# Kernel tuning notes

Hardware: AMD Instinct MI355X
Metric: run time of the kernel (lower is better)

## Reference

```python
import jax, jax.numpy as jnp
import numpy as np

HEADS = 4


def setup_inputs() -> dict:
    key = jax.random.key(0)
    k1, k2, k3, k4 = jax.random.split(key, 4)
    B, C, H, W = 4, 256, 64, 64
    x = jax.random.normal(k1, (B, C, H, W), dtype=jnp.float32)
    w_qkv = jax.random.normal(k2, (3 * C, C), dtype=jnp.float32) * (C ** -0.5)
    w_proj = jax.random.normal(k3, (C, C), dtype=jnp.float32) * (C ** -0.5)
    b_proj = jax.random.normal(k4, (C,), dtype=jnp.float32) * 0.01
    return {"x": x, "w_qkv": w_qkv, "w_proj": w_proj, "b_proj": b_proj}


def reference(x, w_qkv, w_proj, b_proj):
    B, C, H, W = x.shape
    heads = HEADS
    dh = C // heads
    scale = dh ** -0.5
    N = H * W
    # 1x1 conv == channel matmul
    qkv = jnp.einsum('bchw,oc->bohw', x, w_qkv)  # [B, 3C, H, W]
    q, k, v = jnp.split(qkv, 3, axis=1)          # each [B, C, H, W]

    def rs(t):
        # [B, C, H, W] -> [B, heads, N, dh]
        return t.reshape(B, heads, dh, N).transpose(0, 1, 3, 2)

    q, k, v = rs(q), rs(k), rs(v)
    attn = jax.nn.softmax(jnp.einsum('bhnd,bhmd->bhnm', q, k) * scale, axis=-1)
    out = jnp.einsum('bhnm,bhmd->bhnd', attn, v)        # [B, heads, N, dh]
    out = out.transpose(0, 1, 3, 2).reshape(B, C, H, W)  # back to spatial
    return jnp.einsum('bchw,oc->bohw', out, w_proj) + b_proj[None, :, None, None]
```

## Files before the change

kernel.cpp:

```cpp
#include <hip/hip_runtime.h>
#include <hip/hip_bf16.h>

#define NPOS   4096
#define TOTP   16384
#define C      256
#define DH     64

typedef unsigned short ushort_t;
typedef __attribute__((ext_vector_type(8))) short short8;
typedef __attribute__((ext_vector_type(4))) float f32x4;

__device__ __forceinline__ f32x4 mfma16(short8 a, short8 b, f32x4 c) {
  return __builtin_amdgcn_mfma_f32_16x16x32_bf16(a, b, c, 0, 0, 0);
}

__device__ __forceinline__ ushort_t f2bf(float f) {
  union { float f; unsigned int u; } v;
  v.f = f;
  unsigned int r = v.u + 0x7FFFu + ((v.u >> 16) & 1u);
  return (ushort_t)(r >> 16);
}

__device__ __forceinline__ unsigned int pack_bf16x2(float lo, float hi) {
  __hip_bfloat162 h = __float22bfloat162_rn(float2{lo, hi});
  union { __hip_bfloat162 h; unsigned int u; } v;
  v.h = h;
  return v.u;
}

__device__ __forceinline__ float fast_exp2(float x) {
  float r;
  asm("v_exp_f32 %0, %1" : "=v"(r) : "v"(x));
  return r;
}

__global__ __launch_bounds__(256) void pack_w(const float* __restrict__ wq,
                                              const float* __restrict__ wp,
                                              ushort_t* __restrict__ wqb,
                                              ushort_t* __restrict__ wpb) {
  int idx = blockIdx.x * 256 + threadIdx.x;
  if (idx < 49152) {
    float4 v = *(const float4*)(wq + (size_t)idx * 4);
    float sc = (idx * 4 < 65536) ? 0.18033688f : 1.0f;
    ushort_t* d = wqb + (size_t)idx * 4;
    unsigned long long pk =
        (unsigned long long)f2bf(v.x * sc) |
        ((unsigned long long)f2bf(v.y * sc) << 16) |
        ((unsigned long long)f2bf(v.z * sc) << 32) |
        ((unsigned long long)f2bf(v.w * sc) << 48);
    *(unsigned long long*)d = pk;
  } else {
    int j = idx - 49152;
    float4 v = *(const float4*)(wp + (size_t)j * 4);
    ushort_t* d = wpb + (size_t)j * 4;
    unsigned long long pk =
        (unsigned long long)f2bf(v.x) |
        ((unsigned long long)f2bf(v.y) << 16) |
        ((unsigned long long)f2bf(v.z) << 32) |
        ((unsigned long long)f2bf(v.w) << 48);
    *(unsigned long long*)d = pk;
  }
}

__global__ __launch_bounds__(256) void transpose_pack(const float* __restrict__ x,
                                                      ushort_t* __restrict__ xT) {
  __shared__ ushort_t tile[64][68];
  int nb = blockIdx.x * 64, cb = blockIdx.y * 64, b = blockIdx.z;
  int tr = threadIdx.x >> 4;
  int tc = (threadIdx.x & 15) * 4;
  const float* src = x + ((size_t)b * C + cb) * NPOS + nb;
#pragma unroll
  for (int it = 0; it < 4; ++it) {
    int c = tr + it * 16;
    float4 v = *(const float4*)(src + (size_t)c * NPOS + tc);
    tile[c][tc + 0] = f2bf(v.x);
    tile[c][tc + 1] = f2bf(v.y);
    tile[c][tc + 2] = f2bf(v.z);
    tile[c][tc + 3] = f2bf(v.w);
  }
  __syncthreads();
  ushort_t* dst = xT + ((size_t)b * NPOS + nb) * C + cb;
#pragma unroll
  for (int it = 0; it < 4; ++it) {
    int n = tr + it * 16;
    unsigned long long pk =
        (unsigned long long)tile[tc + 0][n] |
        ((unsigned long long)tile[tc + 1][n] << 16) |
        ((unsigned long long)tile[tc + 2][n] << 32) |
        ((unsigned long long)tile[tc + 3][n] << 48);
    *(unsigned long long*)(dst + (size_t)n * C + tc) = pk;
  }
}

__global__ __launch_bounds__(256) void gemm_qk(const ushort_t* __restrict__ xT,
                                               const ushort_t* __restrict__ Wq,
                                               ushort_t* __restrict__ qk) {
  int w = threadIdx.x >> 6, l = threadIdx.x & 63;
  int lr = l & 15, lg = l >> 4;
  int mbase = blockIdx.x * 128 + w * 32;
  int nbase = blockIdx.y * 64;
  f32x4 acc[2][4] = {};
#pragma unroll
  for (int kk = 0; kk < 8; ++kk) {
    short8 a0 = *(const short8*)(xT + (size_t)(mbase + lr) * C + kk * 32 + lg * 8);
    short8 a1 = *(const short8*)(xT + (size_t)(mbase + 16 + lr) * C + kk * 32 + lg * 8);
#pragma unroll
    for (int t = 0; t < 4; ++t) {
      short8 b = *(const short8*)(Wq + (size_t)(nbase + t * 16 + lr) * C + kk * 32 + lg * 8);
      acc[0][t] = mfma16(a0, b, acc[0][t]);
      acc[1][t] = mfma16(a1, b, acc[1][t]);
    }
  }
#pragma unroll
  for (int qq = 0; qq < 2; ++qq)
#pragma unroll
    for (int t = 0; t < 4; ++t)
#pragma unroll
      for (int i = 0; i < 4; ++i)
        qk[(size_t)(mbase + qq * 16 + lg * 4 + i) * 512 + nbase + t * 16 + lr] =
            f2bf(acc[qq][t][i]);
}

__global__ __launch_bounds__(256) void gemm_v(const ushort_t* __restrict__ xT,
                                              const ushort_t* __restrict__ Wq,
                                              ushort_t* __restrict__ vT) {
  int w = threadIdx.x >> 6, l = threadIdx.x & 63;
  int lr = l & 15, lg = l >> 4;
  int obase = blockIdx.y * 128 + w * 32;
  int pbase = blockIdx.x * 64;
  f32x4 acc[2][4] = {};
#pragma unroll
  for (int kk = 0; kk < 8; ++kk) {
    short8 a0 = *(const short8*)(Wq + (size_t)(512 + obase + lr) * C + kk * 32 + lg * 8);
    short8 a1 = *(const short8*)(Wq + (size_t)(512 + obase + 16 + lr) * C + kk * 32 + lg * 8);
#pragma unroll
    for (int t = 0; t < 4; ++t) {
      short8 b = *(const short8*)(xT + (size_t)(pbase + t * 16 + lr) * C + kk * 32 + lg * 8);
      acc[0][t] = mfma16(a0, b, acc[0][t]);
      acc[1][t] = mfma16(a1, b, acc[1][t]);
    }
  }
#pragma unroll
  for (int qq = 0; qq < 2; ++qq)
#pragma unroll
    for (int i = 0; i < 4; ++i) {
      int ov = obase + qq * 16 + lg * 4 + i;
#pragma unroll
      for (int t = 0; t < 4; ++t) {
        int p = pbase + t * 16 + lr;
        vT[((size_t)((p >> 12) * 256 + ov)) * NPOS + (p & 4095)] = f2bf(acc[qq][t][i]);
      }
    }
}

__global__ __launch_bounds__(128, 2) void attn_kernel(const ushort_t* __restrict__ qk,
                                                      const ushort_t* __restrict__ vT,
                                                      ushort_t* __restrict__ ao) {
  __shared__ ushort_t Ks[2][64][64];
  __shared__ ushort_t Vs[2][64][64];
  __shared__ ushort_t Pw[2][2048];

  int tid = threadIdx.x;
  int w = tid >> 6, l = tid & 63;
  int lr = l & 15, lg = l >> 4;

  int bh = blockIdx.y;
  int qtile = blockIdx.x;
  int b = bh >> 2, h = bh & 3;
  size_t bbase = (size_t)b * NPOS;
  int qbase = qtile * 64 + w * 32;

  const ushort_t* qkb = qk + bbase * 512;
  const ushort_t* vTb = vT + ((size_t)(b * 256 + h * DH)) * NPOS;

  const ushort_t* ksrc[4];
  const ushort_t* vsrc[4];
  ushort_t* kdst[4];
  ushort_t* vdst[4];
#pragma unroll
  for (int j = 0; j < 4; ++j) {
    int c = j * 128 + tid;
    int row = c >> 3, slot = c & 7;
    ksrc[j] = qkb + (size_t)row * 512 + 256 + h * DH + slot * 8;
    vsrc[j] = vTb + (size_t)row * NPOS + slot * 8;
    kdst[j] = &Ks[0][row][((slot * 16) ^ (((row >> 2) & 7) << 4)) >> 1];
    vdst[j] = &Vs[0][row][((slot * 16) ^ ((row & 7) << 4)) >> 1];
  }
  short8 gk[4], gv[4];
#pragma unroll
  for (int j = 0; j < 4; ++j) {
    gk[j] = *(const short8*)ksrc[j];
    gv[j] = *(const short8*)vsrc[j];
  }

  short8 aq[2][2];
#pragma unroll
  for (int qq = 0; qq < 2; ++qq)
#pragma unroll
    for (int ks = 0; ks < 2; ++ks)
      aq[qq][ks] = *(const short8*)(qkb + (size_t)(qbase + qq * 16 + lr) * 512 +
                                    h * DH + ks * 32 + lg * 8);

  f32x4 o[2][4] = {};
  float mi[2][4] = {{-1e30f, -1e30f, -1e30f, -1e30f}, {-1e30f, -1e30f, -1e30f, -1e30f}};
  float li[2][4] = {};

  for (int kt = 0; kt < 64; ++kt) {
    int buf = kt & 1;
#pragma unroll
    for (int j = 0; j < 4; ++j) {
      *(short8*)(kdst[j] + buf * 4096) = gk[j];
      *(short8*)(vdst[j] + buf * 4096) = gv[j];
    }
    __syncthreads();

    if (kt < 63) {
#pragma unroll
      for (int j = 0; j < 4; ++j) {
        ksrc[j] += 64 * 512;
        vsrc[j] += 64;
        gk[j] = *(const short8*)ksrc[j];
        gv[j] = *(const short8*)vsrc[j];
      }
    }

    f32x4 s[2][4] = {};
#pragma unroll
    for (int ks = 0; ks < 2; ++ks) {
      short8 bk[4];
#pragma unroll
      for (int t = 0; t < 4; ++t) {
        int row = lr * 4 + t;
        int colb = (ks * 64 + lg * 16) ^ ((lr & 7) << 4);
        bk[t] = *(const short8*)&Ks[buf][row][colb >> 1];
      }
#pragma unroll
      for (int qq = 0; qq < 2; ++qq)
#pragma unroll
        for (int t = 0; t < 4; ++t)
          s[qq][t] = mfma16(aq[qq][ks], bk[t], s[qq][t]);
    }

    float m4[2][4];
    bool bad = false;
#pragma unroll
    for (int qq = 0; qq < 2; ++qq)
#pragma unroll
      for (int i = 0; i < 4; ++i) {
        m4[qq][i] = fmaxf(fmaxf(s[qq][0][i], s[qq][1][i]),
                          fmaxf(s[qq][2][i], s[qq][3][i]));
        bad = bad || (m4[qq][i] > mi[qq][i] + 8.0f);
      }

    if (__any(bad)) {
#pragma unroll
      for (int qq = 0; qq < 2; ++qq)
#pragma unroll
        for (int i = 0; i < 4; ++i) {
          float mx = m4[qq][i];
#pragma unroll
          for (int msk = 1; msk <= 8; msk <<= 1) mx = fmaxf(mx, __shfl_xor(mx, msk, 64));
          float mnew = fmaxf(mi[qq][i], mx);
          float corr = fast_exp2(mi[qq][i] - mnew);
          float p0 = fast_exp2(s[qq][0][i] - mnew);
          float p1 = fast_exp2(s[qq][1][i] - mnew);
          float p2 = fast_exp2(s[qq][2][i] - mnew);
          float p3 = fast_exp2(s[qq][3][i] - mnew);
          li[qq][i] = li[qq][i] * corr + ((p0 + p1) + (p2 + p3));
          mi[qq][i] = mnew;
#pragma unroll
          for (int t = 0; t < 4; ++t) o[qq][t][i] *= corr;
          int r = qq * 16 + lg * 4 + i;
          uint2 pr;
          pr.x = pack_bf16x2(p0, p1);
          pr.y = pack_bf16x2(p2, p3);
          *(uint2*)&Pw[w][r * 64 + ((lr * 4) ^ ((r & 7) << 3))] = pr;
        }
    } else {
#pragma unroll
      for (int qq = 0; qq < 2; ++qq)
#pragma unroll
        for (int i = 0; i < 4; ++i) {
          float m = mi[qq][i];
          float p0 = fast_exp2(s[qq][0][i] - m);
          float p1 = fast_exp2(s[qq][1][i] - m);
          float p2 = fast_exp2(s[qq][2][i] - m);
          float p3 = fast_exp2(s[qq][3][i] - m);
          li[qq][i] += (p0 + p1) + (p2 + p3);
          int r = qq * 16 + lg * 4 + i;
          uint2 pr;
          pr.x = pack_bf16x2(p0, p1);
          pr.y = pack_bf16x2(p2, p3);
          *(uint2*)&Pw[w][r * 64 + ((lr * 4) ^ ((r & 7) << 3))] = pr;
        }
    }

#pragma unroll
    for (int kk = 0; kk < 2; ++kk) {
      short8 bv[4];
#pragma unroll
      for (int t = 0; t < 4; ++t) {
        int row = t * 16 + lr;
        int colb = (kk * 64 + lg * 16) ^ ((row & 7) << 4);
        bv[t] = *(const short8*)&Vs[buf][row][colb >> 1];
      }
#pragma unroll
      for (int qq = 0; qq < 2; ++qq) {
        int r = qq * 16 + lr;
        short8 ap = *(const short8*)&Pw[w][r * 64 + ((kk * 32 + lg * 8) ^ ((r & 7) << 3))];
#pragma unroll
        for (int t = 0; t < 4; ++t) o[qq][t] = mfma16(ap, bv[t], o[qq][t]);
      }
    }
  }

#pragma unroll
  for (int qq = 0; qq < 2; ++qq)
#pragma unroll
    for (int i = 0; i < 4; ++i) {
      float rs = li[qq][i];
#pragma unroll
      for (int msk = 1; msk <= 8; msk <<= 1) rs += __shfl_xor(rs, msk, 64);
      li[qq][i] = rs;
    }

#pragma unroll
  for (int qq = 0; qq < 2; ++qq)
#pragma unroll
    for (int i = 0; i < 4; ++i) {
      float inv = 1.0f / li[qq][i];
      size_t p = bbase + qbase + qq * 16 + lg * 4 + i;
#pragma unroll
      for (int t = 0; t < 4; ++t)
        ao[p * C + h * DH + t * 16 + lr] = f2bf(o[qq][t][i] * inv);
    }
}

__global__ __launch_bounds__(256) void gemm_proj(const ushort_t* __restrict__ ao,
                                                 const ushort_t* __restrict__ Wp,
                                                 const float* __restrict__ bias,
                                                 float* __restrict__ out) {
  int w = threadIdx.x >> 6, l = threadIdx.x & 63;
  int lr = l & 15, lg = l >> 4;
  int obase = blockIdx.y * 128 + w * 32;
  int pbase = blockIdx.x * 64;
  f32x4 acc[2][4] = {};
#pragma unroll
  for (int kk = 0; kk < 8; ++kk) {
    short8 a0 = *(const short8*)(Wp + (size_t)(obase + lr) * C + kk * 32 + lg * 8);
    short8 a1 = *(const short8*)(Wp + (size_t)(obase + 16 + lr) * C + kk * 32 + lg * 8);
#pragma unroll
    for (int t = 0; t < 4; ++t) {
      short8 b = *(const short8*)(ao + (size_t)(pbase + t * 16 + lr) * C + kk * 32 + lg * 8);
      acc[0][t] = mfma16(a0, b, acc[0][t]);
      acc[1][t] = mfma16(a1, b, acc[1][t]);
    }
  }
#pragma unroll
  for (int qq = 0; qq < 2; ++qq)
#pragma unroll
    for (int i = 0; i < 4; ++i) {
      int oc = obase + qq * 16 + lg * 4 + i;
      float bv = bias[oc];
#pragma unroll
      for (int t = 0; t < 4; ++t) {
        int p = pbase + t * 16 + lr;
        out[((size_t)(p >> 12) * C + oc) * NPOS + (p & 4095)] = acc[qq][t][i] + bv;
      }
    }
}

extern "C" void kernel_launch(void* const* d_in, const int* in_sizes, int n_in,
                              void* d_out, int out_size, void* d_ws, size_t ws_size,
                              hipStream_t stream) {
  const float* x      = (const float*)d_in[0];
  const float* w_qkv  = (const float*)d_in[1];
  const float* w_proj = (const float*)d_in[2];
  const float* b_proj = (const float*)d_in[3];
  float* out = (float*)d_out;

  char* ws = (char*)d_ws;
  ushort_t* xT  = (ushort_t*)(ws);
  ushort_t* wqb = (ushort_t*)(ws + 8388608);
  ushort_t* wpb = (ushort_t*)(ws + 8781824);
  ushort_t* qk  = (ushort_t*)(ws + 8912896);
  ushort_t* vT  = (ushort_t*)(ws + 25690112);
  ushort_t* ao  = (ushort_t*)(ws + 34078720);

  pack_w<<<256, 256, 0, stream>>>(w_qkv, w_proj, wqb, wpb);
  transpose_pack<<<dim3(64, 4, 4), 256, 0, stream>>>(x, xT);
  gemm_qk<<<dim3(128, 8), 256, 0, stream>>>(xT, wqb, qk);
  gemm_v<<<dim3(256, 2), 256, 0, stream>>>(xT, wqb, vT);
  attn_kernel<<<dim3(64, 16), 128, 0, stream>>>(qk, vT, ao);
  gemm_proj<<<dim3(256, 2), 256, 0, stream>>>(ao, wpb, b_proj, out);
}
```

Baseline: 189.8 us.

## Make attention blocks single-wave with private single-buffered K/V tiles, no barriers

The attention kernel goes from two waves sharing double-buffered K/V tiles in LDS to one wave per block. Each wave loads its own 64x64 K and V tiles into a single LDS buffer, and the per-iteration __syncthreads is removed. The grid doubles to keep the same number of query rows. This removes block-level barrier stalls, but each wave now fetches the full K/V tiles itself, doubling global/L2 load traffic for K and V. It also doubles the prefetch registers held per thread.

```diff
diff --git a/kernel.cpp b/kernel.cpp
--- a/kernel.cpp
+++ b/kernel.cpp
@@ -153,42 +153,41 @@
     }
 }
 
-__global__ __launch_bounds__(128, 2) void attn_kernel(const ushort_t* __restrict__ qk,
-                                                      const ushort_t* __restrict__ vT,
-                                                      ushort_t* __restrict__ ao) {
-  __shared__ ushort_t Ks[2][64][64];
-  __shared__ ushort_t Vs[2][64][64];
-  __shared__ ushort_t Pw[2][2048];
-
-  int tid = threadIdx.x;
-  int w = tid >> 6, l = tid & 63;
+__global__ __launch_bounds__(64, 2) void attn_kernel(const ushort_t* __restrict__ qk,
+                                                     const ushort_t* __restrict__ vT,
+                                                     ushort_t* __restrict__ ao) {
+  __shared__ ushort_t Ks[64][64];
+  __shared__ ushort_t Vs[64][64];
+  __shared__ ushort_t Pw[2048];
+
+  int l = threadIdx.x;
   int lr = l & 15, lg = l >> 4;
 
   int bh = blockIdx.y;
   int qtile = blockIdx.x;
   int b = bh >> 2, h = bh & 3;
   size_t bbase = (size_t)b * NPOS;
-  int qbase = qtile * 64 + w * 32;
+  int qbase = qtile * 32;
 
   const ushort_t* qkb = qk + bbase * 512;
   const ushort_t* vTb = vT + ((size_t)(b * 256 + h * DH)) * NPOS;
 
-  const ushort_t* ksrc[4];
-  const ushort_t* vsrc[4];
-  ushort_t* kdst[4];
-  ushort_t* vdst[4];
-#pragma unroll
-  for (int j = 0; j < 4; ++j) {
-    int c = j * 128 + tid;
+  const ushort_t* ksrc[8];
+  const ushort_t* vsrc[8];
+  ushort_t* kdst[8];
+  ushort_t* vdst[8];
+#pragma unroll
+  for (int j = 0; j < 8; ++j) {
+    int c = j * 64 + l;
     int row = c >> 3, slot = c & 7;
     ksrc[j] = qkb + (size_t)row * 512 + 256 + h * DH + slot * 8;
     vsrc[j] = vTb + (size_t)row * NPOS + slot * 8;
-    kdst[j] = &Ks[0][row][((slot * 16) ^ (((row >> 2) & 7) << 4)) >> 1];
-    vdst[j] = &Vs[0][row][((slot * 16) ^ ((row & 7) << 4)) >> 1];
-  }
-  short8 gk[4], gv[4];
-#pragma unroll
-  for (int j = 0; j < 4; ++j) {
+    kdst[j] = &Ks[row][((slot * 16) ^ (((row >> 2) & 7) << 4)) >> 1];
+    vdst[j] = &Vs[row][((slot * 16) ^ ((row & 7) << 4)) >> 1];
+  }
+  short8 gk[8], gv[8];
+#pragma unroll
+  for (int j = 0; j < 8; ++j) {
     gk[j] = *(const short8*)ksrc[j];
     gv[j] = *(const short8*)vsrc[j];
   }
@@ -206,17 +205,15 @@
   float li[2][4] = {};
 
   for (int kt = 0; kt < 64; ++kt) {
-    int buf = kt & 1;
-#pragma unroll
-    for (int j = 0; j < 4; ++j) {
-      *(short8*)(kdst[j] + buf * 4096) = gk[j];
-      *(short8*)(vdst[j] + buf * 4096) = gv[j];
-    }
-    __syncthreads();
+#pragma unroll
+    for (int j = 0; j < 8; ++j) {
+      *(short8*)kdst[j] = gk[j];
+      *(short8*)vdst[j] = gv[j];
+    }
 
     if (kt < 63) {
 #pragma unroll
-      for (int j = 0; j < 4; ++j) {
+      for (int j = 0; j < 8; ++j) {
         ksrc[j] += 64 * 512;
         vsrc[j] += 64;
         gk[j] = *(const short8*)ksrc[j];
@@ -232,7 +229,7 @@
       for (int t = 0; t < 4; ++t) {
         int row = lr * 4 + t;
         int colb = (ks * 64 + lg * 16) ^ ((lr & 7) << 4);
-        bk[t] = *(const short8*)&Ks[buf][row][colb >> 1];
+        bk[t] = *(const short8*)&Ks[row][colb >> 1];
       }
 #pragma unroll
       for (int qq = 0; qq < 2; ++qq)
@@ -274,7 +271,7 @@
           uint2 pr;
           pr.x = pack_bf16x2(p0, p1);
           pr.y = pack_bf16x2(p2, p3);
-          *(uint2*)&Pw[w][r * 64 + ((lr * 4) ^ ((r & 7) << 3))] = pr;
+          *(uint2*)&Pw[r * 64 + ((lr * 4) ^ ((r & 7) << 3))] = pr;
         }
     } else {
 #pragma unroll
@@ -291,7 +288,7 @@
           uint2 pr;
           pr.x = pack_bf16x2(p0, p1);
           pr.y = pack_bf16x2(p2, p3);
-          *(uint2*)&Pw[w][r * 64 + ((lr * 4) ^ ((r & 7) << 3))] = pr;
+          *(uint2*)&Pw[r * 64 + ((lr * 4) ^ ((r & 7) << 3))] = pr;
         }
     }
 
@@ -302,12 +299,12 @@
       for (int t = 0; t < 4; ++t) {
         int row = t * 16 + lr;
         int colb = (kk * 64 + lg * 16) ^ ((row & 7) << 4);
-        bv[t] = *(const short8*)&Vs[buf][row][colb >> 1];
+        bv[t] = *(const short8*)&Vs[row][colb >> 1];
       }
 #pragma unroll
       for (int qq = 0; qq < 2; ++qq) {
         int r = qq * 16 + lr;
-        short8 ap = *(const short8*)&Pw[w][r * 64 + ((kk * 32 + lg * 8) ^ ((r & 7) << 3))];
+        short8 ap = *(const short8*)&Pw[r * 64 + ((kk * 32 + lg * 8) ^ ((r & 7) << 3))];
 #pragma unroll
         for (int t = 0; t < 4; ++t) o[qq][t] = mfma16(ap, bv[t], o[qq][t]);
       }
@@ -391,6 +388,6 @@
   transpose_pack<<<dim3(64, 4, 4), 256, 0, stream>>>(x, xT);
   gemm_qk<<<dim3(128, 8), 256, 0, stream>>>(xT, wqb, qk);
   gemm_v<<<dim3(256, 2), 256, 0, stream>>>(xT, wqb, vT);
-  attn_kernel<<<dim3(64, 16), 128, 0, stream>>>(qk, vT, ao);
+  attn_kernel<<<dim3(128, 16), 64, 0, stream>>>(qk, vT, ao);
   gemm_proj<<<dim3(256, 2), 256, 0, stream>>>(ao, wpb, b_proj, out);
 }
```

Result: slower. 372.6 us (+96.4%).
